# Kernel tuning notes

Measured on AMD Instinct MI355X. Metric: run time of the kernel, lower is better.

Reference implementation:

```python
import jax, jax.numpy as jnp
import numpy as np

B, S, H, NH, T = 4, 512, 512, 8, 3
DH = H // NH
DTS = H // T  # 170, per-timescale encoder width
EPS = 1e-5

def _ln(x, g, b):
    m = jnp.mean(x, axis=-1, keepdims=True)
    v = jnp.mean((x - m) ** 2, axis=-1, keepdims=True)
    return (x - m) * jax.lax.rsqrt(v + EPS) * g + b

def _gelu(x):
    return jax.nn.gelu(x, approximate=False)

def _mha(x, qkv_W, qkv_b, out_W, out_b, mask):
    # x: [B,S,H]; qkv_W: [H,3H]; mask: [B,S,S] float additive or None
    qkv = x @ qkv_W + qkv_b
    q, k, v = jnp.split(qkv, 3, axis=-1)
    q = q.reshape(B, S, NH, DH)
    k = k.reshape(B, S, NH, DH)
    v = v.reshape(B, S, NH, DH)
    scores = jnp.einsum('bqhd,bkhd->bhqk', q, k) / jnp.sqrt(jnp.float32(DH))
    if mask is not None:
        scores = scores + mask[:, None, :, :]
    attn = jax.nn.softmax(scores, axis=-1)
    o = jnp.einsum('bhqk,bkhd->bqhd', attn, v).reshape(B, S, H)
    return o @ out_W + out_b

def setup_inputs() -> dict:
    key = jax.random.key(0)
    ks = jax.random.split(key, 32)
    r = lambda i, shape, s=0.02: (jax.random.normal(ks[i], shape, dtype=jnp.float32) * s)
    inp = {}
    inp['x'] = jax.random.normal(ks[0], (B, S, H), dtype=jnp.float32)
    inp['timestamps'] = jax.random.uniform(ks[1], (B, S), dtype=jnp.float32) * 1e6
    # per-timescale encoders (stacked over T)
    inp['enc_W'] = r(2, (T, 2, DTS), 0.5)
    inp['enc_b'] = jnp.zeros((T, DTS), jnp.float32)
    inp['enc_ln_g'] = jnp.ones((T, DTS), jnp.float32)
    inp['enc_ln_b'] = jnp.zeros((T, DTS), jnp.float32)
    # per-timescale MHA
    inp['qkv_W'] = r(3, (T, H, 3 * H))
    inp['qkv_b'] = jnp.zeros((T, 3 * H), jnp.float32)
    inp['attn_out_W'] = r(4, (T, H, H))
    inp['attn_out_b'] = jnp.zeros((T, H), jnp.float32)
    # time mixer
    inp['mixer_W1'] = r(5, (T * H, H))
    inp['mixer_b1'] = jnp.zeros((H,), jnp.float32)
    inp['mixer_ln_g'] = jnp.ones((H,), jnp.float32)
    inp['mixer_ln_b'] = jnp.zeros((H,), jnp.float32)
    inp['mixer_W2'] = r(6, (H, T))
    inp['mixer_b2'] = jnp.zeros((T,), jnp.float32)
    # transformer encoder layer (post-norm, gelu, ffn=4H)
    inp['el_qkv_W'] = r(7, (H, 3 * H))
    inp['el_qkv_b'] = jnp.zeros((3 * H,), jnp.float32)
    inp['el_out_W'] = r(8, (H, H))
    inp['el_out_b'] = jnp.zeros((H,), jnp.float32)
    inp['el_ln1_g'] = jnp.ones((H,), jnp.float32)
    inp['el_ln1_b'] = jnp.zeros((H,), jnp.float32)
    inp['el_ff_W1'] = r(9, (H, 4 * H))
    inp['el_ff_b1'] = jnp.zeros((4 * H,), jnp.float32)
    inp['el_ff_W2'] = r(10, (4 * H, H))
    inp['el_ff_b2'] = jnp.zeros((H,), jnp.float32)
    inp['el_ln2_g'] = jnp.ones((H,), jnp.float32)
    inp['el_ln2_b'] = jnp.zeros((H,), jnp.float32)
    # output projection
    inp['op_W'] = r(11, (H, H))
    inp['op_b'] = jnp.zeros((H,), jnp.float32)
    inp['op_ln_g'] = jnp.ones((H,), jnp.float32)
    inp['op_ln_b'] = jnp.zeros((H,), jnp.float32)
    return inp

def reference(x, timestamps, enc_W, enc_b, enc_ln_g, enc_ln_b, qkv_W, qkv_b, attn_out_W, attn_out_b,
              mixer_W1, mixer_b1, mixer_ln_g, mixer_ln_b, mixer_W2, mixer_b2,
              el_qkv_W, el_qkv_b, el_out_W, el_out_b, el_ln1_g, el_ln1_b,
              el_ff_W1, el_ff_b1, el_ff_W2, el_ff_b2, el_ln2_g, el_ln2_b,
              op_W, op_b, op_ln_g, op_ln_b):
    # pairwise time features [B,S,S]
    time_diff = timestamps[:, :, None] - timestamps[:, None, :]
    direction = jnp.sign(time_diff)
    magnitude = jnp.log1p(jnp.abs(time_diff) / 3600.0)
    outs = []
    for i in range(T):
        mag = magnitude / (10.0 ** i)
        tf = jnp.stack([direction, mag], axis=-1)            # [B,S,S,2]
        e = tf @ enc_W[i] + enc_b[i]                          # [B,S,S,DTS]
        e = _gelu(_ln(e, enc_ln_g[i], enc_ln_b[i]))
        mask = jnp.mean(e, axis=-1)                           # [B,S,S] additive attn mask
        outs.append(_mha(x, qkv_W[i], qkv_b[i], attn_out_W[i], attn_out_b[i], mask))
    combined = jnp.concatenate(outs, axis=-1)                 # [B,S,T*H]
    m = _gelu(_ln(combined @ mixer_W1 + mixer_b1, mixer_ln_g, mixer_ln_b))
    mix = jax.nn.softmax(m @ mixer_W2 + mixer_b2, axis=-1)    # [B,S,T]
    weighted = sum(mix[..., i:i + 1] * outs[i] for i in range(T))
    # post-norm transformer encoder layer
    sa = _mha(weighted, el_qkv_W, el_qkv_b, el_out_W, el_out_b, None)
    h1 = _ln(weighted + sa, el_ln1_g, el_ln1_b)
    ff = _gelu(h1 @ el_ff_W1 + el_ff_b1) @ el_ff_W2 + el_ff_b2
    h2 = _ln(h1 + ff, el_ln2_g, el_ln2_b)
    out = _ln(h2 @ op_W + op_b, op_ln_g, op_ln_b)
    return out
```

## Files before the change

### kernel.cpp

```cpp
#include <hip/hip_runtime.h>
#include <hip/hip_bf16.h>
#include <math.h>

#define Bq 4
#define Sq 512
#define Hq 512
#define NHq 8
#define Tq 3
#define DTSq 170
#define BSq 2048
#define ENCSTRIDE 520
#define NLUT 2048
#define MAGMAXf 5.6304994f

typedef float f32x4 __attribute__((ext_vector_type(4)));
typedef __bf16 bf16x4 __attribute__((ext_vector_type(4)));
typedef __bf16 bf16x8 __attribute__((ext_vector_type(8)));

__device__ __forceinline__ float gelu_f(float x){
  return 0.5f * x * (1.0f + erff(x * 0.70710678118654752f));
}

__device__ __forceinline__ void gload16(const void* g, void* l){
  __builtin_amdgcn_global_load_lds((const __attribute__((address_space(1))) void*)g,
                                   (__attribute__((address_space(3))) void*)l, 16, 0, 0);
}

__device__ __forceinline__ float waveReduceSum(float v){
  #pragma unroll
  for (int off = 32; off > 0; off >>= 1) v += __shfl_xor(v, off);
  return v;
}

__device__ __forceinline__ float blockReduce(float v, float* red){
  int tid = threadIdx.x;
  __syncthreads();
  red[tid] = v; __syncthreads();
  for (int s = 128; s > 0; s >>= 1){
    if (tid < s) red[tid] += red[tid + s];
    __syncthreads();
  }
  return red[0];
}

__global__ __launch_bounds__(256) void enc_prep(const float* __restrict__ encW,
                                                const float* __restrict__ encB,
                                                float* __restrict__ out){
  int t = blockIdx.x, tid = threadIdx.x;
  __shared__ float red[256];
  const float* W0 = encW + t * 2 * DTSq;
  const float* W1 = W0 + DTSq;
  const float* Bv = encB + t * DTSq;
  float w0 = (tid < DTSq) ? W0[tid] : 0.f;
  float w1 = (tid < DTSq) ? W1[tid] : 0.f;
  float bv = (tid < DTSq) ? Bv[tid] : 0.f;
  const float invD = 1.0f / (float)DTSq;
  float m0 = blockReduce(w0, red) * invD;
  float m1 = blockReduce(w1, red) * invD;
  float mb = blockReduce(bv, red) * invD;
  float c0 = (tid < DTSq) ? (w0 - m0) : 0.f;
  float c1 = (tid < DTSq) ? (w1 - m1) : 0.f;
  float cb = (tid < DTSq) ? (bv - mb) : 0.f;
  float* op = out + t * ENCSTRIDE;
  if (tid < DTSq){
    op[tid] = c0; op[DTSq + tid] = c1; op[2 * DTSq + tid] = cb;
  }
  float pa = blockReduce(c0 * c0, red) * invD;
  float pb = blockReduce(c1 * c1, red) * invD;
  float pc = blockReduce(c0 * c1, red) * invD;
  float pd = blockReduce(c0 * cb, red) * invD;
  float pe = blockReduce(c1 * cb, red) * invD;
  float pf = blockReduce(cb * cb, red) * invD;
  if (tid == 0){
    op[3 * DTSq + 0] = pa; op[3 * DTSq + 1] = pb; op[3 * DTSq + 2] = pc;
    op[3 * DTSq + 3] = pd; op[3 * DTSq + 4] = pe; op[3 * DTSq + 5] = pf;
  }
}

__global__ __launch_bounds__(256) void mask_lut_build(const float* __restrict__ enc,
                                                      const float* __restrict__ g,
                                                      const float* __restrict__ be,
                                                      float* __restrict__ lut){
  int td = blockIdx.x;
  int t = td / 3, dsel = td % 3;
  float d = (float)(dsel - 1);
  __shared__ float sw0[DTSq], sw1[DTSq], sbc[DTSq], sg[DTSq], sbe[DTSq];
  const float* ep = enc + t * ENCSTRIDE;
  for (int c = threadIdx.x; c < DTSq; c += 256){
    sw0[c] = ep[c]; sw1[c] = ep[DTSq + c]; sbc[c] = ep[2 * DTSq + c];
    sg[c] = g[t * DTSq + c]; sbe[c] = be[t * DTSq + c];
  }
  __syncthreads();
  float A  = ep[3 * DTSq + 0], Bs = ep[3 * DTSq + 1], Cs = ep[3 * DTSq + 2];
  float Ds = ep[3 * DTSq + 3], Es = ep[3 * DTSq + 4], Fs = ep[3 * DTSq + 5];
  int e = blockIdx.y * 256 + threadIdx.x;
  float tscale = (t == 0) ? 1.f : ((t == 1) ? 0.1f : 0.01f);
  float m = (MAGMAXf / (float)(NLUT - 1)) * (float)e * tscale;
  float var = fabsf(d) * A + m * m * Bs + Fs + 2.f * (d * m * Cs + d * Ds + m * Es);
  float rs = rsqrtf(var + 1e-5f);
  float sum = 0.f;
  for (int c = 0; c < DTSq; ++c){
    float ee = fmaf(m, sw1[c], fmaf(d, sw0[c], sbc[c]));
    float n = fmaf(ee * rs, sg[c], sbe[c]);
    sum += n * 0.5f * (1.0f + erff(n * 0.70710678118654752f));
  }
  lut[td * NLUT + e] = sum * (1.0f / (float)DTSq);
}

__global__ __launch_bounds__(256) void mask_fill(const float* __restrict__ ts,
                                                 const float* __restrict__ lut,
                                                 __bf16* __restrict__ maskbuf){
  int bi = blockIdx.x;
  int b = bi >> 9, i = bi & 511;
  float tsi = ts[bi];
  for (int j0 = 0; j0 < Sq; j0 += 256){
    int j = j0 + threadIdx.x;
    float dt = tsi - ts[(b << 9) + j];
    int dsel = (dt > 0.f) ? 2 : ((dt < 0.f) ? 0 : 1);
    float mag = log1pf(fabsf(dt) * (1.0f / 3600.0f));
    float u = mag * ((float)(NLUT - 1) / MAGMAXf);
    int i0 = (int)u; if (i0 > NLUT - 2) i0 = NLUT - 2;
    float f = u - (float)i0;
    #pragma unroll
    for (int t = 0; t < Tq; ++t){
      const float* lp = lut + (t * 3 + dsel) * NLUT + i0;
      float v = lp[0] + f * (lp[1] - lp[0]);
      maskbuf[(((size_t)(t * Bq + b) * Sq + i) * Sq) + j] = (__bf16)v;
    }
  }
}

struct CvtEnt { const float* W; __bf16* WT; int ldw, ldt, ntn, start; };
struct CvtArgs { CvtEnt e[12]; };

__global__ __launch_bounds__(256) void cvt_wT_all(CvtArgs a){
  int bid = blockIdx.x;
  int i = 0;
  #pragma unroll
  for (int k = 1; k < 12; ++k) if (bid >= a.e[k].start) i = k;
  const float* W = a.e[i].W;
  __bf16* WT = a.e[i].WT;
  int ldw = a.e[i].ldw, ldt = a.e[i].ldt;
  int local = bid - a.e[i].start;
  int tn = local % a.e[i].ntn, tk = local / a.e[i].ntn;
  int n0 = tn * 64, k0 = tk * 64;
  __shared__ float T[64][65];
  int tid = threadIdx.x;
  #pragma unroll
  for (int q = 0; q < 16; ++q){
    int lin = q * 256 + tid;
    int r = lin >> 6, c = lin & 63;
    T[r][c] = W[(size_t)(k0 + r) * ldw + n0 + c];
  }
  __syncthreads();
  #pragma unroll
  for (int q = 0; q < 16; ++q){
    int lin = q * 256 + tid;
    int n = lin >> 6, k = lin & 63;
    WT[(size_t)(n0 + n) * ldt + k0 + k] = (__bf16)T[k][n];
  }
}

__global__ __launch_bounds__(256) void cvt_bf(const float* __restrict__ in,
                                              __bf16* __restrict__ out, int n){
  int idx = (blockIdx.x * 256 + threadIdx.x) * 4;
  if (idx < n){
    float4 v = *(const float4*)&in[idx];
    bf16x4 r; r[0]=(__bf16)v.x; r[1]=(__bf16)v.y; r[2]=(__bf16)v.z; r[3]=(__bf16)v.w;
    *(bf16x4*)&out[idx] = r;
  }
}

template<int BM>
__global__ __launch_bounds__(256) void gemm_pipe(
    const __bf16* __restrict__ A, int lda, size_t sAz,
    const __bf16* __restrict__ BT, int ldb, size_t sBz,
    const float* __restrict__ bias, int sBiasz,
    float* __restrict__ C32, __bf16* __restrict__ C16, int ldc, size_t sCz,
    int K, int act)
{
  constexpr int MF = BM / 32;
  constexpr int ABYTES = BM * 128;
  constexpr int BBYTES = 64 * 128;
  __shared__ __bf16 lds[(2 * (ABYTES + BBYTES)) / 2];
  int tid = threadIdx.x;

  int gx = gridDim.x, nwg = gx * gridDim.y;
  int lin = blockIdx.x + gx * blockIdx.y;
  int q8 = nwg >> 3;
  int swz = (lin & 7) * q8 + (lin >> 3);
  int bx = swz % gx, by = swz / gx;

  int z = blockIdx.z;
  A  += (size_t)z * sAz;
  BT += (size_t)z * sBz;
  const float* bz = bias ? bias + (size_t)z * sBiasz : nullptr;
  size_t cbase = (size_t)z * sCz;
  int brow = by * BM, bcol = bx * 64;

  int lane = tid & 63, w = tid >> 6;
  int wr = (w >> 1) * (BM / 2), wc = (w & 1) * 32;
  int lr = lane & 15, lg = lane >> 4;

  f32x4 acc[MF][2];
  #pragma unroll
  for (int m = 0; m < MF; ++m)
    #pragma unroll
    for (int n = 0; n < 2; ++n) acc[m][n] = (f32x4){0.f, 0.f, 0.f, 0.f};

  char* lbase = (char*)lds;

  auto stage = [&](int buf, int ko){
    char* ab = lbase + buf * (ABYTES + BBYTES);
    #pragma unroll
    for (int qq = 0; qq < BM / 32; ++qq){
      int byte = (qq * 256 + tid) * 16;
      int row = byte >> 7, col8 = byte & 127;
      int src = col8 ^ ((row & 7) << 4);
      gload16(&A[(size_t)(brow + row) * lda + ko + (src >> 1)], ab + byte);
    }
    char* bb = ab + ABYTES;
    #pragma unroll
    for (int qq = 0; qq < 2; ++qq){
      int byte = (qq * 256 + tid) * 16;
      int row = byte >> 7, col8 = byte & 127;
      int src = col8 ^ ((row & 7) << 4);
      gload16(&BT[(size_t)(bcol + row) * ldb + ko + (src >> 1)], bb + byte);
    }
  };

  stage(0, 0);
  int nk = K >> 6;
  for (int kt = 0; kt < nk; ++kt){
    int cur = kt & 1;
    if (kt + 1 < nk){
      stage(cur ^ 1, (kt + 1) << 6);
      if constexpr (BM == 64) asm volatile("s_waitcnt vmcnt(4)" ::: "memory");
      else                    asm volatile("s_waitcnt vmcnt(6)" ::: "memory");
    } else {
      asm volatile("s_waitcnt vmcnt(0)" ::: "memory");
    }
    __builtin_amdgcn_s_barrier();
    __builtin_amdgcn_sched_barrier(0);
    char* ab = lbase + cur * (ABYTES + BBYTES);
    char* bb = ab + ABYTES;
    #pragma unroll
    for (int s = 0; s < 2; ++s){
      bf16x8 af[MF], bfr[2];
      #pragma unroll
      for (int m = 0; m < MF; ++m){
        int row = wr + m * 16 + lr;
        int col8 = (s * 64 + lg * 16) ^ ((row & 7) << 4);
        af[m] = *(const bf16x8*)(ab + row * 128 + col8);
      }
      #pragma unroll
      for (int n = 0; n < 2; ++n){
        int row = wc + n * 16 + lr;
        int col8 = (s * 64 + lg * 16) ^ ((row & 7) << 4);
        bfr[n] = *(const bf16x8*)(bb + row * 128 + col8);
      }
      #pragma unroll
      for (int m = 0; m < MF; ++m)
        #pragma unroll
        for (int n = 0; n < 2; ++n)
          acc[m][n] = __builtin_amdgcn_mfma_f32_16x16x32_bf16(af[m], bfr[n], acc[m][n], 0, 0, 0);
    }
    asm volatile("" ::: "memory");
    __builtin_amdgcn_s_barrier();
  }

  #pragma unroll
  for (int m = 0; m < MF; ++m){
    #pragma unroll
    for (int n = 0; n < 2; ++n){
      int col = bcol + wc + n * 16 + lr;
      float bv = bz ? bz[col] : 0.f;
      #pragma unroll
      for (int j = 0; j < 4; ++j){
        int row = brow + wr + m * 16 + lg * 4 + j;
        float v = acc[m][n][j] + bv;
        if (act) v = gelu_f(v);
        size_t idx = cbase + (size_t)row * ldc + col;
        if (C32) C32[idx] = v;
        if (C16) C16[idx] = (__bf16)v;
      }
    }
  }
}

__global__ __launch_bounds__(256) void flash_attn(
    const __bf16* __restrict__ qkv, size_t sQz,
    const __bf16* __restrict__ vt,  size_t sVz,
    const __bf16* __restrict__ mask, size_t sMz,
    __bf16* __restrict__ ctx, size_t sCz)
{
  int t = blockIdx.z;
  qkv += (size_t)t * sQz;
  vt  += (size_t)t * sVz;
  ctx += (size_t)t * sCz;
  const __bf16* mk = mask ? mask + (size_t)t * sMz : nullptr;

  int lin = blockIdx.x + (blockIdx.y << 3);
  int swz = (lin & 7) * 32 + (lin >> 3);
  int io = (swz & 7) * 64;
  int bh = swz >> 3;
  int b = bh >> 3, h = bh & 7;

  __shared__ __bf16 Qs[64][72], Ks[64][72], Vs[64][72];
  __shared__ __bf16 Ps[4][16][72];
  int tid = threadIdx.x, lane = tid & 63, w = tid >> 6;
  int lr = lane & 15, lg = lane >> 4;

  #pragma unroll
  for (int q = 0; q < 2; ++q){
    int linr = q * 256 + tid;
    int r = linr >> 3, c0 = (linr & 7) * 8;
    *(bf16x8*)&Qs[r][c0] = *(const bf16x8*)&qkv[(size_t)(b * Sq + io + r) * 1536 + h * 64 + c0];
  }

  f32x4 o[4];
  #pragma unroll
  for (int n = 0; n < 4; ++n) o[n] = (f32x4){0.f, 0.f, 0.f, 0.f};
  float mrow[4] = {-1e30f, -1e30f, -1e30f, -1e30f};
  float lrow[4] = {0.f, 0.f, 0.f, 0.f};

  for (int jo = 0; jo < Sq; jo += 64){
    __syncthreads();
    #pragma unroll
    for (int q = 0; q < 2; ++q){
      int linr = q * 256 + tid;
      int r = linr >> 3, c0 = (linr & 7) * 8;
      *(bf16x8*)&Ks[r][c0] = *(const bf16x8*)&qkv[(size_t)(b * Sq + jo + r) * 1536 + 512 + h * 64 + c0];
      *(bf16x8*)&Vs[r][c0] = *(const bf16x8*)&vt[((size_t)bh * 64 + r) * Sq + jo + c0];
    }
    __syncthreads();

    f32x4 s4[4];
    #pragma unroll
    for (int n = 0; n < 4; ++n) s4[n] = (f32x4){0.f, 0.f, 0.f, 0.f};
    #pragma unroll
    for (int s = 0; s < 2; ++s){
      bf16x8 af = *(const bf16x8*)&Qs[w * 16 + lr][s * 32 + lg * 8];
      #pragma unroll
      for (int n = 0; n < 4; ++n){
        bf16x8 bfr = *(const bf16x8*)&Ks[n * 16 + lr][s * 32 + lg * 8];
        s4[n] = __builtin_amdgcn_mfma_f32_16x16x32_bf16(af, bfr, s4[n], 0, 0, 0);
      }
    }

    float sv[4][4];
    #pragma unroll
    for (int n = 0; n < 4; ++n){
      #pragma unroll
      for (int reg = 0; reg < 4; ++reg){
        float v = s4[n][reg] * 0.125f;
        if (mk){
          int irow = io + w * 16 + lg * 4 + reg;
          v += (float)mk[((size_t)b * Sq + irow) * Sq + jo + n * 16 + lr];
        }
        sv[n][reg] = v;
      }
    }

    #pragma unroll
    for (int reg = 0; reg < 4; ++reg){
      float pmax = fmaxf(fmaxf(sv[0][reg], sv[1][reg]), fmaxf(sv[2][reg], sv[3][reg]));
      #pragma unroll
      for (int off = 1; off < 16; off <<= 1) pmax = fmaxf(pmax, __shfl_xor(pmax, off));
      float mnew = fmaxf(mrow[reg], pmax);
      float corr = __expf(mrow[reg] - mnew);
      mrow[reg] = mnew;
      float rs = 0.f;
      #pragma unroll
      for (int n = 0; n < 4; ++n){
        float p = __expf(sv[n][reg] - mnew);
        sv[n][reg] = p;
        rs += p;
      }
      #pragma unroll
      for (int off = 1; off < 16; off <<= 1) rs += __shfl_xor(rs, off);
      lrow[reg] = lrow[reg] * corr + rs;
      #pragma unroll
      for (int n = 0; n < 4; ++n) o[n][reg] *= corr;
    }

    #pragma unroll
    for (int n = 0; n < 4; ++n)
      #pragma unroll
      for (int reg = 0; reg < 4; ++reg)
        Ps[w][lg * 4 + reg][n * 16 + lr] = (__bf16)sv[n][reg];
    #pragma unroll
    for (int s = 0; s < 2; ++s){
      bf16x8 af = *(const bf16x8*)&Ps[w][lr][s * 32 + lg * 8];
      #pragma unroll
      for (int n = 0; n < 4; ++n){
        bf16x8 bfr = *(const bf16x8*)&Vs[n * 16 + lr][s * 32 + lg * 8];
        o[n] = __builtin_amdgcn_mfma_f32_16x16x32_bf16(af, bfr, o[n], 0, 0, 0);
      }
    }
  }

  #pragma unroll
  for (int reg = 0; reg < 4; ++reg){
    float inv = 1.0f / lrow[reg];
    int row = b * Sq + io + w * 16 + lg * 4 + reg;
    #pragma unroll
    for (int n = 0; n < 4; ++n)
      ctx[(size_t)row * Hq + h * 64 + n * 16 + lr] = (__bf16)(o[n][reg] * inv);
  }
}

__global__ __launch_bounds__(256) void ln_rows(const float* __restrict__ in,
                                               const float* __restrict__ res,
                                               const float* __restrict__ g,
                                               const float* __restrict__ bb,
                                               float* __restrict__ out32,
                                               __bf16* __restrict__ out16,
                                               int do_gelu){
  int row = blockIdx.x * 4 + (threadIdx.x >> 6);
  int lane = threadIdx.x & 63;
  const float* ir = in + (size_t)row * Hq;
  const float* rr = res ? res + (size_t)row * Hq : nullptr;
  float x[8]; float s = 0.f, sq = 0.f;
  #pragma unroll
  for (int k = 0; k < 8; ++k){
    int c = lane + 64 * k;
    float v = ir[c];
    if (rr) v += rr[c];
    x[k] = v; s += v; sq += v * v;
  }
  s = waveReduceSum(s); sq = waveReduceSum(sq);
  float mean = s * (1.0f / Hq);
  float var = fmaxf(sq * (1.0f / Hq) - mean * mean, 0.f);
  float rstd = rsqrtf(var + 1e-5f);
  #pragma unroll
  for (int k = 0; k < 8; ++k){
    int c = lane + 64 * k;
    float y = (x[k] - mean) * rstd * g[c] + bb[c];
    if (do_gelu) y = gelu_f(y);
    if (out32) out32[(size_t)row * Hq + c] = y;
    if (out16) out16[(size_t)row * Hq + c] = (__bf16)y;
  }
}

__global__ __launch_bounds__(256) void ln_mixer_weighted(const float* __restrict__ in,
                                                         const float* __restrict__ g,
                                                         const float* __restrict__ bb,
                                                         const float* __restrict__ W2,
                                                         const float* __restrict__ b2,
                                                         const __bf16* __restrict__ comb,
                                                         float* __restrict__ out32,
                                                         __bf16* __restrict__ out16){
  int row = blockIdx.x * 4 + (threadIdx.x >> 6);
  int lane = threadIdx.x & 63;
  const float* ir = in + (size_t)row * Hq;
  float x[8]; float s = 0.f, sq = 0.f;
  #pragma unroll
  for (int k = 0; k < 8; ++k){
    int c = lane + 64 * k;
    float v = ir[c];
    x[k] = v; s += v; sq += v * v;
  }
  s = waveReduceSum(s); sq = waveReduceSum(sq);
  float mean = s * (1.0f / Hq);
  float var = fmaxf(sq * (1.0f / Hq) - mean * mean, 0.f);
  float rstd = rsqrtf(var + 1e-5f);
  float a0 = 0.f, a1 = 0.f, a2 = 0.f;
  #pragma unroll
  for (int k = 0; k < 8; ++k){
    int c = lane + 64 * k;
    float y = gelu_f((x[k] - mean) * rstd * g[c] + bb[c]);
    const float* wv = W2 + c * 3;
    a0 = fmaf(y, wv[0], a0); a1 = fmaf(y, wv[1], a1); a2 = fmaf(y, wv[2], a2);
  }
  a0 = waveReduceSum(a0) + b2[0];
  a1 = waveReduceSum(a1) + b2[1];
  a2 = waveReduceSum(a2) + b2[2];
  float mx = fmaxf(a0, fmaxf(a1, a2));
  float e0 = __expf(a0 - mx), e1 = __expf(a1 - mx), e2 = __expf(a2 - mx);
  float inv = 1.0f / (e0 + e1 + e2);
  float m0 = e0 * inv, m1 = e1 * inv, m2 = e2 * inv;
  const __bf16* cr = comb + (size_t)row * 1536;
  #pragma unroll
  for (int k = 0; k < 8; ++k){
    int c = lane + 64 * k;
    float v = m0 * (float)cr[c] + m1 * (float)cr[512 + c] + m2 * (float)cr[1024 + c];
    out32[(size_t)row * Hq + c] = v;
    out16[(size_t)row * Hq + c] = (__bf16)v;
  }
}

__global__ __launch_bounds__(256) void transpose_v(const __bf16* __restrict__ qkv, size_t sQz,
                                                   __bf16* __restrict__ vt, size_t sVz){
  int t = blockIdx.z;
  qkv += (size_t)t * sQz;
  vt  += (size_t)t * sVz;
  int bh = blockIdx.y, b = bh >> 3, h = bh & 7;
  int so = blockIdx.x * 64;
  __shared__ __bf16 T[64][72];
  int tid = threadIdx.x;
  #pragma unroll
  for (int q = 0; q < 16; ++q){
    int lin = q * 256 + tid;
    int r = lin >> 6, c = lin & 63;
    T[r][c] = qkv[(size_t)(b * Sq + so + r) * 1536 + 1024 + h * 64 + c];
  }
  __syncthreads();
  #pragma unroll
  for (int q = 0; q < 16; ++q){
    int lin = q * 256 + tid;
    int d = lin >> 6, s = lin & 63;
    vt[((size_t)bh * 64 + d) * Sq + so + s] = T[s][d];
  }
}

extern "C" void kernel_launch(void* const* d_in, const int* in_sizes, int n_in,
                              void* d_out, int out_size, void* d_ws, size_t ws_size,
                              hipStream_t stream){
  const float* x         = (const float*)d_in[0];
  const float* ts        = (const float*)d_in[1];
  const float* enc_W     = (const float*)d_in[2];
  const float* enc_b     = (const float*)d_in[3];
  const float* enc_ln_g  = (const float*)d_in[4];
  const float* enc_ln_b  = (const float*)d_in[5];
  const float* qkv_W     = (const float*)d_in[6];
  const float* qkv_b     = (const float*)d_in[7];
  const float* aout_W    = (const float*)d_in[8];
  const float* aout_b    = (const float*)d_in[9];
  const float* mx_W1     = (const float*)d_in[10];
  const float* mx_b1     = (const float*)d_in[11];
  const float* mx_ln_g   = (const float*)d_in[12];
  const float* mx_ln_b   = (const float*)d_in[13];
  const float* mx_W2     = (const float*)d_in[14];
  const float* mx_b2     = (const float*)d_in[15];
  const float* el_qkv_W  = (const float*)d_in[16];
  const float* el_qkv_b  = (const float*)d_in[17];
  const float* el_out_W  = (const float*)d_in[18];
  const float* el_out_b  = (const float*)d_in[19];
  const float* el_ln1_g  = (const float*)d_in[20];
  const float* el_ln1_b  = (const float*)d_in[21];
  const float* el_ff_W1  = (const float*)d_in[22];
  const float* el_ff_b1  = (const float*)d_in[23];
  const float* el_ff_W2  = (const float*)d_in[24];
  const float* el_ff_b2  = (const float*)d_in[25];
  const float* el_ln2_g  = (const float*)d_in[26];
  const float* el_ln2_b  = (const float*)d_in[27];
  const float* op_W      = (const float*)d_in[28];
  const float* op_b      = (const float*)d_in[29];
  const float* op_ln_g   = (const float*)d_in[30];
  const float* op_ln_b   = (const float*)d_in[31];

  float* ws = (float*)d_ws;
  size_t o = 0;
  __bf16* MASKBb = (__bf16*)(ws + o); o += 1572864;
  __bf16* XB     = (__bf16*)(ws + o); o += 524288;
  __bf16* qkvT   = (__bf16*)(ws + o); o += 1179648;
  __bf16* aoutT  = (__bf16*)(ws + o); o += 393216;
  __bf16* mx1T   = (__bf16*)(ws + o); o += 393216;
  __bf16* elqkvT = (__bf16*)(ws + o); o += 393216;
  __bf16* eloutT = (__bf16*)(ws + o); o += 131072;
  __bf16* ff1T   = (__bf16*)(ws + o); o += 524288;
  __bf16* ff2T   = (__bf16*)(ws + o); o += 524288;
  __bf16* opT    = (__bf16*)(ws + o); o += 131072;
  __bf16* QKVb   = (__bf16*)(ws + o); o += 4718592;
  __bf16* VTb    = (__bf16*)(ws + o); o += 1572864;
  __bf16* FFBb   = (__bf16*)(ws + o); o += 2097152;
  __bf16* CTXb   = (__bf16*)(ws + o); o += 1572864;
  __bf16* COMBb  = (__bf16*)(ws + o); o += 1572864;
  float*  MBUF   = ws + o;            o += 1048576;
  float*  WEI    = ws + o;            o += 1048576;
  __bf16* WEIb   = (__bf16*)(ws + o); o += 524288;
  float*  SA     = ws + o;            o += 1048576;
  float*  H1     = ws + o;            o += 1048576;
  __bf16* H1b    = (__bf16*)(ws + o); o += 524288;
  float*  H2     = ws + o;            o += 1048576;
  __bf16* H2b    = (__bf16*)(ws + o); o += 524288;
  float*  ENC    = ws + o;            o += 1600;
  float*  LUTB   = ws + o;            o += 9 * NLUT;
  float*  OPO    = MBUF;

  cvt_bf<<<1024, 256, 0, stream>>>(x, XB, BSq * Hq);
  {
    CvtArgs ca;
    for (int t = 0; t < 3; ++t)
      ca.e[t] = {qkv_W + (size_t)t * 512 * 1536, qkvT + (size_t)t * 1536 * 512, 1536, 512, 24, 192 * t};
    for (int t = 0; t < 3; ++t)
      ca.e[3 + t] = {aout_W + (size_t)t * 512 * 512, aoutT + (size_t)t * 512 * 512, 512, 512, 8, 576 + 64 * t};
    ca.e[6]  = {mx_W1,    mx1T,   512,  1536, 8,  768};
    ca.e[7]  = {el_qkv_W, elqkvT, 1536, 512,  24, 960};
    ca.e[8]  = {el_out_W, eloutT, 512,  512,  8,  1152};
    ca.e[9]  = {el_ff_W1, ff1T,   2048, 512,  32, 1216};
    ca.e[10] = {el_ff_W2, ff2T,   512,  2048, 8,  1472};
    ca.e[11] = {op_W,     opT,    512,  512,  8,  1728};
    cvt_wT_all<<<1792, 256, 0, stream>>>(ca);
  }

  enc_prep<<<Tq, 256, 0, stream>>>(enc_W, enc_b, ENC);
  mask_lut_build<<<dim3(9, NLUT / 256), 256, 0, stream>>>(ENC, enc_ln_g, enc_ln_b, LUTB);
  mask_fill<<<BSq, 256, 0, stream>>>(ts, LUTB, MASKBb);

  gemm_pipe<128><<<dim3(24, 16, 3), 256, 0, stream>>>(XB, 512, 0, qkvT, 512, (size_t)1536 * 512,
      qkv_b, 1536, nullptr, QKVb, 1536, (size_t)2048 * 1536, 512, 0);
  transpose_v<<<dim3(8, 32, 3), 256, 0, stream>>>(QKVb, (size_t)2048 * 1536, VTb, (size_t)32 * 64 * 512);
  flash_attn<<<dim3(8, 32, 3), 256, 0, stream>>>(QKVb, (size_t)2048 * 1536,
      VTb, (size_t)32 * 64 * 512, MASKBb, (size_t)4 * 512 * 512, CTXb, (size_t)2048 * 512);
  gemm_pipe<64><<<dim3(8, 32, 3), 256, 0, stream>>>(CTXb, 512, (size_t)2048 * 512, aoutT, 512, (size_t)512 * 512,
      aout_b, 512, nullptr, COMBb, 1536, 512, 512, 0);

  gemm_pipe<64><<<dim3(8, 32, 1), 256, 0, stream>>>(COMBb, 1536, 0, mx1T, 1536, 0,
      mx_b1, 0, MBUF, nullptr, 512, 0, 1536, 0);
  ln_mixer_weighted<<<512, 256, 0, stream>>>(MBUF, mx_ln_g, mx_ln_b, mx_W2, mx_b2, COMBb, WEI, WEIb);

  gemm_pipe<128><<<dim3(24, 16, 1), 256, 0, stream>>>(WEIb, 512, 0, elqkvT, 512, 0,
      el_qkv_b, 0, nullptr, QKVb, 1536, 0, 512, 0);
  transpose_v<<<dim3(8, 32, 1), 256, 0, stream>>>(QKVb, 0, VTb, 0);
  flash_attn<<<dim3(8, 32, 1), 256, 0, stream>>>(QKVb, 0, VTb, 0, nullptr, 0, CTXb, 0);
  gemm_pipe<64><<<dim3(8, 32, 1), 256, 0, stream>>>(CTXb, 512, 0, eloutT, 512, 0,
      el_out_b, 0, SA, nullptr, 512, 0, 512, 0);
  ln_rows<<<512, 256, 0, stream>>>(WEI, SA, el_ln1_g, el_ln1_b, H1, H1b, 0);
  gemm_pipe<128><<<dim3(32, 16, 1), 256, 0, stream>>>(H1b, 512, 0, ff1T, 512, 0,
      el_ff_b1, 0, nullptr, FFBb, 2048, 0, 512, 1);
  gemm_pipe<64><<<dim3(8, 32, 1), 256, 0, stream>>>(FFBb, 2048, 0, ff2T, 2048, 0,
      el_ff_b2, 0, SA, nullptr, 512, 0, 2048, 0);
  ln_rows<<<512, 256, 0, stream>>>(H1, SA, el_ln2_g, el_ln2_b, H2, H2b, 0);

  gemm_pipe<64><<<dim3(8, 32, 1), 256, 0, stream>>>(H2b, 512, 0, opT, 512, 0,
      op_b, 0, OPO, nullptr, 512, 0, 512, 0);
  ln_rows<<<512, 256, 0, stream>>>(OPO, nullptr, op_ln_g, op_ln_b, (float*)d_out, nullptr, 0);
}
```

Measured before the change: 226.6 us.

## Double-buffer K/V tiles in flash attention via async LDS loads with swizzle

```diff
diff --git a/kernel.cpp b/kernel.cpp
--- a/kernel.cpp
+++ b/kernel.cpp
@@ -288,6 +288,7 @@
   }
 }
 
+template<bool HM>
 __global__ __launch_bounds__(256) void flash_attn(
     const __bf16* __restrict__ qkv, size_t sQz,
     const __bf16* __restrict__ vt,  size_t sVz,
@@ -298,7 +299,7 @@
   qkv += (size_t)t * sQz;
   vt  += (size_t)t * sVz;
   ctx += (size_t)t * sCz;
-  const __bf16* mk = mask ? mask + (size_t)t * sMz : nullptr;
+  const __bf16* mk = HM ? mask + (size_t)t * sMz : nullptr;
 
   int lin = blockIdx.x + (blockIdx.y << 3);
   int swz = (lin & 7) * 32 + (lin >> 3);
@@ -306,17 +307,35 @@
   int bh = swz >> 3;
   int b = bh >> 3, h = bh & 7;
 
-  __shared__ __bf16 Qs[64][72], Ks[64][72], Vs[64][72];
+  constexpr int KB = 64 * 128;
+  __shared__ __bf16 lds[(2 * 2 * KB) / 2];
   __shared__ __bf16 Ps[4][16][72];
   int tid = threadIdx.x, lane = tid & 63, w = tid >> 6;
   int lr = lane & 15, lg = lane >> 4;
 
-  #pragma unroll
-  for (int q = 0; q < 2; ++q){
-    int linr = q * 256 + tid;
-    int r = linr >> 3, c0 = (linr & 7) * 8;
-    *(bf16x8*)&Qs[r][c0] = *(const bf16x8*)&qkv[(size_t)(b * Sq + io + r) * 1536 + h * 64 + c0];
-  }
+  const __bf16* qrow = &qkv[(size_t)(b * Sq + io + w * 16 + lr) * 1536 + h * 64];
+  bf16x8 q0 = *(const bf16x8*)&qrow[lg * 8];
+  bf16x8 q1 = *(const bf16x8*)&qrow[32 + lg * 8];
+
+  char* lb = (char*)lds;
+  auto stage = [&](int buf, int jo){
+    char* kb = lb + buf * (2 * KB);
+    #pragma unroll
+    for (int qq = 0; qq < 2; ++qq){
+      int byte = (qq * 256 + tid) * 16;
+      int row = byte >> 7, col8 = byte & 127;
+      int src = col8 ^ ((row & 7) << 4);
+      gload16(&qkv[(size_t)(b * Sq + jo + row) * 1536 + 512 + h * 64 + (src >> 1)], kb + byte);
+    }
+    char* vb = kb + KB;
+    #pragma unroll
+    for (int qq = 0; qq < 2; ++qq){
+      int byte = (qq * 256 + tid) * 16;
+      int row = byte >> 7, col8 = byte & 127;
+      int src = col8 ^ ((row & 7) << 4);
+      gload16(&vt[((size_t)bh * 64 + row) * Sq + jo + (src >> 1)], vb + byte);
+    }
+  };
 
   f32x4 o[4];
   #pragma unroll
@@ -324,64 +343,80 @@
   float mrow[4] = {-1e30f, -1e30f, -1e30f, -1e30f};
   float lrow[4] = {0.f, 0.f, 0.f, 0.f};
 
-  for (int jo = 0; jo < Sq; jo += 64){
-    __syncthreads();
-    #pragma unroll
-    for (int q = 0; q < 2; ++q){
-      int linr = q * 256 + tid;
-      int r = linr >> 3, c0 = (linr & 7) * 8;
-      *(bf16x8*)&Ks[r][c0] = *(const bf16x8*)&qkv[(size_t)(b * Sq + jo + r) * 1536 + 512 + h * 64 + c0];
-      *(bf16x8*)&Vs[r][c0] = *(const bf16x8*)&vt[((size_t)bh * 64 + r) * Sq + jo + c0];
-    }
-    __syncthreads();
+  stage(0, 0);
+  #pragma unroll
+  for (int kt = 0; kt < 8; ++kt){
+    int cur = kt & 1;
+    int jo = kt << 6;
+
+    float mv[4][4];
+    if (HM){
+      #pragma unroll
+      for (int n = 0; n < 4; ++n)
+        #pragma unroll
+        for (int reg = 0; reg < 4; ++reg)
+          mv[n][reg] = (float)mk[((size_t)(b * Sq + io + w * 16 + lg * 4 + reg)) * Sq + jo + n * 16 + lr];
+    }
+
+    if (kt + 1 < 8){
+      stage(cur ^ 1, (kt + 1) << 6);
+      if (HM) asm volatile("s_waitcnt vmcnt(20)" ::: "memory");
+      else    asm volatile("s_waitcnt vmcnt(4)"  ::: "memory");
+    } else {
+      asm volatile("s_waitcnt vmcnt(0)" ::: "memory");
+    }
+    __builtin_amdgcn_s_barrier();
+    __builtin_amdgcn_sched_barrier(0);
+
+    char* kb = lb + cur * (2 * KB);
+    char* vb = kb + KB;
 
     f32x4 s4[4];
     #pragma unroll
     for (int n = 0; n < 4; ++n) s4[n] = (f32x4){0.f, 0.f, 0.f, 0.f};
+    __builtin_amdgcn_s_setprio(1);
     #pragma unroll
     for (int s = 0; s < 2; ++s){
-      bf16x8 af = *(const bf16x8*)&Qs[w * 16 + lr][s * 32 + lg * 8];
+      bf16x8 aq = s ? q1 : q0;
       #pragma unroll
       for (int n = 0; n < 4; ++n){
-        bf16x8 bfr = *(const bf16x8*)&Ks[n * 16 + lr][s * 32 + lg * 8];
-        s4[n] = __builtin_amdgcn_mfma_f32_16x16x32_bf16(af, bfr, s4[n], 0, 0, 0);
+        int row = n * 16 + lr;
+        int colb = (s * 64 + lg * 16) ^ ((row & 7) << 4);
+        bf16x8 bk = *(const bf16x8*)(kb + row * 128 + colb);
+        s4[n] = __builtin_amdgcn_mfma_f32_16x16x32_bf16(aq, bk, s4[n], 0, 0, 0);
       }
     }
+    __builtin_amdgcn_s_setprio(0);
 
     float sv[4][4];
     #pragma unroll
-    for (int n = 0; n < 4; ++n){
-      #pragma unroll
-      for (int reg = 0; reg < 4; ++reg){
-        float v = s4[n][reg] * 0.125f;
-        if (mk){
-          int irow = io + w * 16 + lg * 4 + reg;
-          v += (float)mk[((size_t)b * Sq + irow) * Sq + jo + n * 16 + lr];
-        }
-        sv[n][reg] = v;
-      }
-    }
+    for (int n = 0; n < 4; ++n)
+      #pragma unroll
+      for (int reg = 0; reg < 4; ++reg)
+        sv[n][reg] = s4[n][reg] * 0.125f + (HM ? mv[n][reg] : 0.f);
 
     #pragma unroll
     for (int reg = 0; reg < 4; ++reg){
       float pmax = fmaxf(fmaxf(sv[0][reg], sv[1][reg]), fmaxf(sv[2][reg], sv[3][reg]));
       #pragma unroll
       for (int off = 1; off < 16; off <<= 1) pmax = fmaxf(pmax, __shfl_xor(pmax, off));
-      float mnew = fmaxf(mrow[reg], pmax);
-      float corr = __expf(mrow[reg] - mnew);
-      mrow[reg] = mnew;
+      if (pmax > mrow[reg] + 8.0f){
+        float corr = __expf(mrow[reg] - pmax);
+        mrow[reg] = pmax;
+        lrow[reg] *= corr;
+        #pragma unroll
+        for (int n = 0; n < 4; ++n) o[n][reg] *= corr;
+      }
       float rs = 0.f;
       #pragma unroll
       for (int n = 0; n < 4; ++n){
-        float p = __expf(sv[n][reg] - mnew);
+        float p = __expf(sv[n][reg] - mrow[reg]);
         sv[n][reg] = p;
         rs += p;
       }
       #pragma unroll
       for (int off = 1; off < 16; off <<= 1) rs += __shfl_xor(rs, off);
-      lrow[reg] = lrow[reg] * corr + rs;
-      #pragma unroll
-      for (int n = 0; n < 4; ++n) o[n][reg] *= corr;
+      lrow[reg] += rs;
     }
 
     #pragma unroll
@@ -389,15 +424,22 @@
       #pragma unroll
       for (int reg = 0; reg < 4; ++reg)
         Ps[w][lg * 4 + reg][n * 16 + lr] = (__bf16)sv[n][reg];
+    __builtin_amdgcn_s_setprio(1);
     #pragma unroll
     for (int s = 0; s < 2; ++s){
-      bf16x8 af = *(const bf16x8*)&Ps[w][lr][s * 32 + lg * 8];
+      bf16x8 ap = *(const bf16x8*)&Ps[w][lr][s * 32 + lg * 8];
       #pragma unroll
       for (int n = 0; n < 4; ++n){
-        bf16x8 bfr = *(const bf16x8*)&Vs[n * 16 + lr][s * 32 + lg * 8];
-        o[n] = __builtin_amdgcn_mfma_f32_16x16x32_bf16(af, bfr, o[n], 0, 0, 0);
+        int row = n * 16 + lr;
+        int colb = (s * 64 + lg * 16) ^ ((row & 7) << 4);
+        bf16x8 bv = *(const bf16x8*)(vb + row * 128 + colb);
+        o[n] = __builtin_amdgcn_mfma_f32_16x16x32_bf16(ap, bv, o[n], 0, 0, 0);
       }
     }
+    __builtin_amdgcn_s_setprio(0);
+
+    asm volatile("" ::: "memory");
+    __builtin_amdgcn_s_barrier();
   }
 
   #pragma unroll
@@ -602,7 +644,7 @@
   gemm_pipe<128><<<dim3(24, 16, 3), 256, 0, stream>>>(XB, 512, 0, qkvT, 512, (size_t)1536 * 512,
       qkv_b, 1536, nullptr, QKVb, 1536, (size_t)2048 * 1536, 512, 0);
   transpose_v<<<dim3(8, 32, 3), 256, 0, stream>>>(QKVb, (size_t)2048 * 1536, VTb, (size_t)32 * 64 * 512);
-  flash_attn<<<dim3(8, 32, 3), 256, 0, stream>>>(QKVb, (size_t)2048 * 1536,
+  flash_attn<true><<<dim3(8, 32, 3), 256, 0, stream>>>(QKVb, (size_t)2048 * 1536,
       VTb, (size_t)32 * 64 * 512, MASKBb, (size_t)4 * 512 * 512, CTXb, (size_t)2048 * 512);
   gemm_pipe<64><<<dim3(8, 32, 3), 256, 0, stream>>>(CTXb, 512, (size_t)2048 * 512, aoutT, 512, (size_t)512 * 512,
       aout_b, 512, nullptr, COMBb, 1536, 512, 512, 0);
@@ -614,7 +656,7 @@
   gemm_pipe<128><<<dim3(24, 16, 1), 256, 0, stream>>>(WEIb, 512, 0, elqkvT, 512, 0,
       el_qkv_b, 0, nullptr, QKVb, 1536, 0, 512, 0);
   transpose_v<<<dim3(8, 32, 1), 256, 0, stream>>>(QKVb, 0, VTb, 0);
-  flash_attn<<<dim3(8, 32, 1), 256, 0, stream>>>(QKVb, 0, VTb, 0, nullptr, 0, CTXb, 0);
+  flash_attn<false><<<dim3(8, 32, 1), 256, 0, stream>>>(QKVb, 0, VTb, 0, nullptr, 0, CTXb, 0);
   gemm_pipe<64><<<dim3(8, 32, 1), 256, 0, stream>>>(CTXb, 512, 0, eloutT, 512, 0,
       el_out_b, 0, SA, nullptr, 512, 0, 512, 0);
   ln_rows<<<512, 256, 0, stream>>>(WEI, SA, el_ln1_g, el_ln1_b, H1, H1b, 0);
```

Measured after the change: 217.0 us. 1.04x faster.
